# Performance work log

Measured on AMD Instinct MI355X. Metric: run time of the kernel, lower is better.

The kernel has to match this reference:

```python
import jax, jax.numpy as jnp
import numpy as np
from jax.scipy.linalg import expm

B, T = 32, 4096
FREQ_DIM = 128
HID = 64
OUT_DIM = 2
N_COMP = 4
DT = 0.1
EPS = 1e-5


def setup_inputs() -> dict:
    key = jax.random.key(0)
    ks = jax.random.split(key, 16)
    f32 = jnp.float32

    def lin(k, out_d, in_d):
        bound = 1.0 / np.sqrt(in_d)
        kw, kb = jax.random.split(k)
        W = jax.random.uniform(kw, (out_d, in_d), f32, -bound, bound)
        b = jax.random.uniform(kb, (out_d,), f32, -bound, bound)
        return W, b

    x = jax.random.normal(ks[0], (B, T, 1), f32)
    # EnhancedWavePhysics params
    freq_spectrum = jnp.linspace(1.0, 20.0, FREQ_DIM, dtype=f32)
    pm_w1, pm_b1 = lin(ks[1], 128, 1)
    pm_w2, pm_b2 = lin(ks[2], FREQ_DIM * 2, 128)
    wc_w, wc_b = lin(ks[3], HID, FREQ_DIM)
    amp_ctrl = jnp.ones((1,), f32) * 0.1
    # quantum encoder
    qe_w1, qe_b1 = lin(ks[4], HID * 2, HID)
    qe_w2, qe_b2 = lin(ks[5], HID * 4, HID * 2)
    # layernorm
    ln_g = jnp.ones((HID * 4,), f32)
    ln_b = jnp.zeros((HID * 4,), f32)
    # skew-symmetric hamiltonians [4, 64, 64]
    A = jax.random.normal(ks[6], (N_COMP, HID, HID), f32) * 0.05
    hams = (A - jnp.swapaxes(A, -1, -2)) / 2.0
    # interference net
    int_w1, int_b1 = lin(ks[7], 32, 4)
    int_w2, int_b2 = lin(ks[8], OUT_DIM, 32)
    int_strength = jnp.ones((1,), f32)
    return dict(x=x, freq_spectrum=freq_spectrum, pm_w1=pm_w1, pm_b1=pm_b1,
                pm_w2=pm_w2, pm_b2=pm_b2, wc_w=wc_w, wc_b=wc_b,
                amp_ctrl=amp_ctrl, qe_w1=qe_w1, qe_b1=qe_b1, qe_w2=qe_w2,
                qe_b2=qe_b2, ln_g=ln_g, ln_b=ln_b, hams=hams,
                int_w1=int_w1, int_b1=int_b1, int_w2=int_w2, int_b2=int_b2,
                int_strength=int_strength)


def reference(x, freq_spectrum, pm_w1, pm_b1, pm_w2, pm_b2, wc_w, wc_b,
              amp_ctrl, qe_w1, qe_b1, qe_w2, qe_b2, ln_g, ln_b, hams,
              int_w1, int_b1, int_w2, int_b2, int_strength):
    Bx, Tx, _ = x.shape
    # --- EnhancedWavePhysics ---
    mod = jnp.tanh(x @ pm_w1.T + pm_b1) @ pm_w2.T + pm_b2            # [B,T,2F]
    amplitude, phase = jnp.split(mod, 2, axis=-1)                     # [B,T,F]
    amplitude = jnp.tanh(amplitude) * amp_ctrl
    time = jnp.linspace(0.0, 2.0 * np.pi, Tx)[None, :, None]          # [1,T,1]
    freqs = freq_spectrum[None, None, :]                              # [1,1,F]
    wave_components = amplitude * jnp.sin(freqs * time + phase)       # [B,T,F]
    wave_field = jnp.tanh(wave_components @ wc_w.T + wc_b)            # [B,T,H]
    # --- quantum encoder + layernorm ---
    q = jnp.tanh(wave_field @ qe_w1.T + qe_b1) @ qe_w2.T + qe_b2      # [B,T,4H]
    mu = q.mean(-1, keepdims=True)
    var = q.var(-1, keepdims=True)
    q = (q - mu) / jnp.sqrt(var + EPS) * ln_g + ln_b
    psi = q.reshape(Bx, Tx, N_COMP, HID)                              # [B,T,C,D]
    # --- Hamiltonian evolution: torch does matrix_exp(-1j*(1j*H)*dt)=expm(H*dt)
    #     (H skew-symmetric real => U real orthogonal), then psi @ U.T, take real.
    U = jax.vmap(expm)(hams * DT)                                     # [C,D,D]
    evolved = jnp.einsum('btcd,ced->btce', psi, U)                    # [B,T,C,D]
    # --- EnhancedInterference ---
    spec = jnp.abs(jnp.fft.fft(evolved, axis=1))                      # [B,T,C,D]
    freq_w = jax.nn.softmax(spec.mean(-1), axis=1)                    # [B,T,C]
    weighted = jnp.sum(spec * freq_w[..., None], axis=1)              # [B,C,D]
    spatial_avg = weighted.mean(-1)                                   # [B,C]
    out = jnp.tanh(spatial_avg @ int_w1.T + int_b1) @ int_w2.T + int_b2
    return out * int_strength                                         # [B,out_dim]
```

## Files before the change

kernel.cpp:

```cpp
#include <hip/hip_runtime.h>
#include <hip/hip_bf16.h>

#define TT 4096
#define BB 32

typedef unsigned short ushort_t;
typedef __attribute__((ext_vector_type(8))) short short8v;
typedef __attribute__((ext_vector_type(4))) float float4v;

__device__ inline ushort_t bf16rn(float v) {
    unsigned u = __float_as_uint(v);
    unsigned r = (u + 0x7FFFu + ((u >> 16) & 1u)) >> 16;
    return (ushort_t)r;
}
__device__ inline float bf16tof(ushort_t h) {
    return __uint_as_float(((unsigned)h) << 16);
}
__device__ inline int SW(int i) { return i + (i >> 5); }

__device__ inline float fast_tanh(float x) {
    float e = __builtin_amdgcn_exp2f(x * 2.8853900817779268f);
    return 1.0f - 2.0f * __builtin_amdgcn_rcpf(e + 1.0f);
}
__device__ inline float fast_sin(float x) {
    return __builtin_amdgcn_sinf(x * 0.15915494309189535f);
}

__global__ __launch_bounds__(256) void k1_expm(const float* __restrict__ hams,
                                               float* __restrict__ U)
{
    int c = blockIdx.x, tid = threadIdx.x;
    __shared__ float M[4096], P[4096], Acc[4096];
    const float* H = hams + c * 4096;
    for (int k = tid; k < 4096; k += 256) {
        float m = H[k] * 0.1f;
        M[k] = m; P[k] = m;
        Acc[k] = m + (((k >> 6) == (k & 63)) ? 1.0f : 0.0f);
    }
    __syncthreads();
    int j = tid & 63;
    float mcol[64];
    #pragma unroll
    for (int k = 0; k < 64; k++) mcol[k] = M[k * 64 + j];
    for (int term = 2; term <= 8; term++) {
        float inv = 1.0f / (float)term;
        float np_[16];
        #pragma unroll
        for (int r = 0; r < 16; r++) {
            int i = (tid >> 6) + 4 * r;
            float a = 0.f;
            #pragma unroll
            for (int k = 0; k < 64; k++) a = fmaf(P[i * 64 + k], mcol[k], a);
            np_[r] = a * inv;
        }
        __syncthreads();
        #pragma unroll
        for (int r = 0; r < 16; r++) {
            int i = (tid >> 6) + 4 * r;
            P[i * 64 + j] = np_[r];
            Acc[i * 64 + j] += np_[r];
        }
        __syncthreads();
    }
    for (int k = tid; k < 4096; k += 256) U[c * 4096 + k] = Acc[k];
}

__global__ void split_all(const float* __restrict__ pw2, const float* __restrict__ wcw,
                          const float* __restrict__ qw1, const float* __restrict__ qw2,
                          ushort_t* __restrict__ wb)
{
    int i = blockIdx.x * 256 + threadIdx.x;
    const float* src; ushort_t *hi, *lo; int off;
    if (i < 32768)      { src = pw2; hi = wb;          lo = wb + 32768;  off = i; }
    else if (i < 40960) { src = wcw; hi = wb + 65536;  lo = wb + 73728;  off = i - 32768; }
    else if (i < 49152) { src = qw1; hi = wb + 81920;  lo = wb + 90112;  off = i - 40960; }
    else                { src = qw2; hi = wb + 98304;  lo = wb + 131072; off = i - 49152; }
    float v = src[off];
    ushort_t h = bf16rn(v);
    hi[off] = h;
    lo[off] = bf16rn(v - bf16tof(h));
}

template<int EPI>
__global__ __launch_bounds__(256, 2) void gemm_v2(
    const ushort_t* __restrict__ Ahi, const ushort_t* __restrict__ Alo,
    const ushort_t* __restrict__ Whi, const ushort_t* __restrict__ Wlo,
    const float* __restrict__ bias,
    const float* __restrict__ x, const float* __restrict__ pw1,
    const float* __restrict__ pb1,
    const float* __restrict__ freq, const float* __restrict__ ampc,
    const float* __restrict__ lng, const float* __restrict__ lnb,
    ushort_t* __restrict__ OHi, ushort_t* __restrict__ OLo,
    float* __restrict__ OF)
{
    __shared__ float partS[2][4][16], partSS[2][4][16];
    int tid = threadIdx.x;
    int w = tid >> 6, l = tid & 63, l15 = l & 15, kg = l >> 4;
    int kofb = kg * 8;

    short8v bh[4][4], bl[4][4];
    #pragma unroll
    for (int i = 0; i < 4; i++) {
        int n = (w + 4 * i) * 16 + l15;
        #pragma unroll
        for (int kc = 0; kc < 4; kc++) {
            int kof = kc * 32 + kofb;
            bh[i][kc] = *(const short8v*)(Whi + (size_t)n * 128 + kof);
            bl[i][kc] = *(const short8v*)(Wlo + (size_t)n * 128 + kof);
        }
    }

    float fr[2], ba[2], bp[2], am = 0.f;
    float bv[4], g4[4], be4[4];
    if (EPI == 1) {
        am = ampc[0];
        #pragma unroll
        for (int i = 0; i < 2; i++) {
            int f = (w + 4 * i) * 16 + l15;
            fr[i] = freq[f]; ba[i] = bias[f]; bp[i] = bias[128 + f];
        }
    } else {
        #pragma unroll
        for (int i = 0; i < 4; i++) {
            int n = (w + 4 * i) * 16 + l15;
            bv[i] = bias[n]; g4[i] = lng[n]; be4[i] = lnb[n];
        }
    }

    int mbase = blockIdx.x * 64;
    for (int mi = 0; mi < 4; mi++) {
        int m0 = mbase + mi * 16;
        short8v ah[4], al[4];
        if (EPI == 1) {
            float xv = x[m0 + l15];
            #pragma unroll
            for (int kc = 0; kc < 4; kc++) {
                int k0 = kc * 32 + kofb;
                float4 w0 = *(const float4*)(pw1 + k0);
                float4 w1v = *(const float4*)(pw1 + k0 + 4);
                float4 b0 = *(const float4*)(pb1 + k0);
                float4 b1v = *(const float4*)(pb1 + k0 + 4);
                #pragma unroll
                for (int j = 0; j < 8; j++) {
                    float wj = (j < 4) ? (&w0.x)[j] : (&w1v.x)[j - 4];
                    float bj = (j < 4) ? (&b0.x)[j] : (&b1v.x)[j - 4];
                    float v = fast_tanh(fmaf(xv, wj, bj));
                    ushort_t h = bf16rn(v);
                    ah[kc][j] = (short)h;
                    al[kc][j] = (short)bf16rn(v - bf16tof(h));
                }
            }
        } else {
            #pragma unroll
            for (int kc = 0; kc < 4; kc++) {
                int kof = kc * 32 + kofb;
                ah[kc] = *(const short8v*)(Ahi + (size_t)(m0 + l15) * 128 + kof);
                al[kc] = *(const short8v*)(Alo + (size_t)(m0 + l15) * 128 + kof);
            }
        }

        float4v acc[4];
        #pragma unroll
        for (int i = 0; i < 4; i++) acc[i] = (float4v){0.f, 0.f, 0.f, 0.f};
        #pragma unroll
        for (int kc = 0; kc < 4; kc++) {
            #pragma unroll
            for (int i = 0; i < 4; i++) {
                acc[i] = __builtin_amdgcn_mfma_f32_16x16x32_bf16(ah[kc], bh[i][kc], acc[i], 0, 0, 0);
                acc[i] = __builtin_amdgcn_mfma_f32_16x16x32_bf16(ah[kc], bl[i][kc], acc[i], 0, 0, 0);
                acc[i] = __builtin_amdgcn_mfma_f32_16x16x32_bf16(al[kc], bh[i][kc], acc[i], 0, 0, 0);
            }
        }

        if (EPI == 1) {
            #pragma unroll
            for (int i = 0; i < 2; i++) {
                int f = (w + 4 * i) * 16 + l15;
                #pragma unroll
                for (int r = 0; r < 4; r++) {
                    int m = m0 + kg * 4 + r;
                    float timev = 6.283185307179586f * (float)(m & 4095) / 4095.0f;
                    float a = fast_tanh(acc[i][r] + ba[i]) * am;
                    float ph = acc[i + 2][r] + bp[i];
                    float v = a * fast_sin(fmaf(fr[i], timev, ph));
                    ushort_t h = bf16rn(v);
                    OHi[(size_t)m * 128 + f] = h;
                    OLo[(size_t)m * 128 + f] = bf16rn(v - bf16tof(h));
                }
            }
        } else {
            float s[4] = {0, 0, 0, 0}, ss[4] = {0, 0, 0, 0};
            #pragma unroll
            for (int i = 0; i < 4; i++) {
                #pragma unroll
                for (int r = 0; r < 4; r++) {
                    float v = acc[i][r] + bv[i];
                    s[r] += v; ss[r] += v * v;
                }
            }
            #pragma unroll
            for (int r = 0; r < 4; r++) {
                #pragma unroll
                for (int off = 1; off < 16; off <<= 1) {
                    s[r] += __shfl_xor(s[r], off);
                    ss[r] += __shfl_xor(ss[r], off);
                }
            }
            int pb_ = mi & 1;
            if (l15 == 0) {
                #pragma unroll
                for (int r = 0; r < 4; r++) {
                    partS[pb_][w][kg * 4 + r] = s[r];
                    partSS[pb_][w][kg * 4 + r] = ss[r];
                }
            }
            __syncthreads();
            float mu[4], rstd[4];
            #pragma unroll
            for (int r = 0; r < 4; r++) {
                float ts = 0.f, tss = 0.f;
                #pragma unroll
                for (int wv = 0; wv < 4; wv++) {
                    ts += partS[pb_][wv][kg * 4 + r];
                    tss += partSS[pb_][wv][kg * 4 + r];
                }
                mu[r] = ts * (1.0f / 256.0f);
                float var = tss * (1.0f / 256.0f) - mu[r] * mu[r];
                rstd[r] = rsqrtf(var + 1e-5f);
            }
            int b = m0 >> 12;
            int t0 = (m0 & 4095) + kg * 4;
            unsigned* OU = (unsigned*)OF;
            #pragma unroll
            for (int i = 0; i < 4; i++) {
                int n = (w + 4 * i) * 16 + l15;
                uint4 ov;
                #pragma unroll
                for (int r = 0; r < 4; r++) {
                    float v = (acc[i][r] + bv[i] - mu[r]) * rstd[r] * g4[i] + be4[i];
                    ushort_t h = bf16rn(v);
                    ushort_t lo2 = bf16rn(v - bf16tof(h));
                    (&ov.x)[r] = (unsigned)h | ((unsigned)lo2 << 16);
                }
                *(uint4*)(OU + (((size_t)b * 256 + n) << 12) + t0) = ov;
            }
        }
    }
}

__global__ __launch_bounds__(256, 2) void s23_v2(
    const ushort_t* __restrict__ Ahi, const ushort_t* __restrict__ Alo,
    const ushort_t* __restrict__ W2hi, const ushort_t* __restrict__ W2lo,
    const float* __restrict__ b2,
    const ushort_t* __restrict__ W3hi, const ushort_t* __restrict__ W3lo,
    const float* __restrict__ b3,
    ushort_t* __restrict__ OHi, ushort_t* __restrict__ OLo)
{
    __shared__ unsigned WF[2][16][65];
    int tid = threadIdx.x;
    int w = tid >> 6, l = tid & 63, l15 = l & 15, kg = l >> 4;
    int kofb = kg * 8;

    short8v w2h[4], w2l[4];
    #pragma unroll
    for (int kc = 0; kc < 4; kc++) {
        int n = w * 16 + l15;
        int kof = kc * 32 + kofb;
        w2h[kc] = *(const short8v*)(W2hi + (size_t)n * 128 + kof);
        w2l[kc] = *(const short8v*)(W2lo + (size_t)n * 128 + kof);
    }
    short8v w3h[2][2], w3l[2][2];
    #pragma unroll
    for (int i = 0; i < 2; i++) {
        int n = (w + 4 * i) * 16 + l15;
        #pragma unroll
        for (int kc = 0; kc < 2; kc++) {
            int kof = kc * 32 + kofb;
            w3h[i][kc] = *(const short8v*)(W3hi + (size_t)n * 64 + kof);
            w3l[i][kc] = *(const short8v*)(W3lo + (size_t)n * 64 + kof);
        }
    }
    float b2v = b2[w * 16 + l15];
    float b3v[2];
    #pragma unroll
    for (int i = 0; i < 2; i++) b3v[i] = b3[(w + 4 * i) * 16 + l15];

    int mbase = blockIdx.x * 64;
    for (int mi = 0; mi < 4; mi++) {
        int m0 = mbase + mi * 16;
        short8v ah[4], al[4];
        #pragma unroll
        for (int kc = 0; kc < 4; kc++) {
            int kof = kc * 32 + kofb;
            ah[kc] = *(const short8v*)(Ahi + (size_t)(m0 + l15) * 128 + kof);
            al[kc] = *(const short8v*)(Alo + (size_t)(m0 + l15) * 128 + kof);
        }
        float4v acc1 = (float4v){0.f, 0.f, 0.f, 0.f};
        #pragma unroll
        for (int kc = 0; kc < 4; kc++) {
            acc1 = __builtin_amdgcn_mfma_f32_16x16x32_bf16(ah[kc], w2h[kc], acc1, 0, 0, 0);
            acc1 = __builtin_amdgcn_mfma_f32_16x16x32_bf16(ah[kc], w2l[kc], acc1, 0, 0, 0);
            acc1 = __builtin_amdgcn_mfma_f32_16x16x32_bf16(al[kc], w2h[kc], acc1, 0, 0, 0);
        }
        int buf = mi & 1;
        #pragma unroll
        for (int r = 0; r < 4; r++) {
            float v = fast_tanh(acc1[r] + b2v);
            ushort_t h = bf16rn(v);
            ushort_t lo2 = bf16rn(v - bf16tof(h));
            WF[buf][kg * 4 + r][w * 16 + l15] = (unsigned)h | ((unsigned)lo2 << 16);
        }
        __syncthreads();
        float4v acc2[2];
        acc2[0] = (float4v){0.f, 0.f, 0.f, 0.f};
        acc2[1] = (float4v){0.f, 0.f, 0.f, 0.f};
        #pragma unroll
        for (int kc = 0; kc < 2; kc++) {
            short8v a2h, a2l;
            #pragma unroll
            for (int j = 0; j < 8; j++) {
                unsigned u = WF[buf][l15][kc * 32 + kofb + j];
                a2h[j] = (short)(u & 0xFFFFu);
                a2l[j] = (short)(u >> 16);
            }
            #pragma unroll
            for (int i = 0; i < 2; i++) {
                acc2[i] = __builtin_amdgcn_mfma_f32_16x16x32_bf16(a2h, w3h[i][kc], acc2[i], 0, 0, 0);
                acc2[i] = __builtin_amdgcn_mfma_f32_16x16x32_bf16(a2h, w3l[i][kc], acc2[i], 0, 0, 0);
                acc2[i] = __builtin_amdgcn_mfma_f32_16x16x32_bf16(a2l, w3h[i][kc], acc2[i], 0, 0, 0);
            }
        }
        #pragma unroll
        for (int i = 0; i < 2; i++) {
            int n = (w + 4 * i) * 16 + l15;
            #pragma unroll
            for (int r = 0; r < 4; r++) {
                int m = m0 + kg * 4 + r;
                float v = fast_tanh(acc2[i][r] + b3v[i]);
                ushort_t h = bf16rn(v);
                OHi[(size_t)m * 128 + n] = h;
                OLo[(size_t)m * 128 + n] = bf16rn(v - bf16tof(h));
            }
        }
    }
}

__global__ __launch_bounds__(256) void k3a_mfma(float* __restrict__ psi,
                                                const float* __restrict__ U)
{
    __shared__ unsigned QP[64 * 261];
    int bid = blockIdx.x;
    int b = bid >> 6, c = (bid >> 4) & 3, tc = bid & 15;
    int t0 = tc * 256;
    int tid = threadIdx.x;
    int w = tid >> 6, l = tid & 63;
    int l15 = l & 15, kq = l >> 4;
    size_t gbase = ((size_t)(b * 256 + c * 64)) * TT + t0;
    const unsigned* psiu = (const unsigned*)psi;

    for (int i = 0; i < 16; i++) {
        int r_ = i * 4 + w;
        int t4 = l * 4;
        uint4 v = *(const uint4*)(psiu + gbase + (size_t)r_ * TT + t4);
        QP[r_ * 261 + t4 + 0] = v.x;
        QP[r_ * 261 + t4 + 1] = v.y;
        QP[r_ * 261 + t4 + 2] = v.z;
        QP[r_ * 261 + t4 + 3] = v.w;
    }
    __syncthreads();

    short8v ua_hi[2], ua_lo[2];
    #pragma unroll
    for (int kc = 0; kc < 2; kc++) {
        #pragma unroll
        for (int j = 0; j < 8; j++) {
            float v = U[c * 4096 + (w * 16 + l15) * 64 + kc * 32 + kq * 8 + j];
            ushort_t h = bf16rn(v);
            ua_hi[kc][j] = (short)h;
            ua_lo[kc][j] = (short)bf16rn(v - bf16tof(h));
        }
    }

    for (int nt = 0; nt < 16; nt++) {
        float4v acc = (float4v){0.f, 0.f, 0.f, 0.f};
        #pragma unroll
        for (int kc = 0; kc < 2; kc++) {
            short8v b_hi, b_lo;
            #pragma unroll
            for (int j = 0; j < 8; j++) {
                unsigned u = QP[(kc * 32 + kq * 8 + j) * 261 + nt * 16 + l15];
                b_hi[j] = (short)(u & 0xFFFFu);
                b_lo[j] = (short)(u >> 16);
            }
            acc = __builtin_amdgcn_mfma_f32_16x16x32_bf16(ua_hi[kc], b_hi, acc, 0, 0, 0);
            acc = __builtin_amdgcn_mfma_f32_16x16x32_bf16(ua_hi[kc], b_lo, acc, 0, 0, 0);
            acc = __builtin_amdgcn_mfma_f32_16x16x32_bf16(ua_lo[kc], b_hi, acc, 0, 0, 0);
        }
        #pragma unroll
        for (int r = 0; r < 4; r++) {
            int e = w * 16 + kq * 4 + r;
            psi[gbase + (size_t)e * TT + nt * 16 + l15] = acc[r];
        }
    }
}

__global__ __launch_bounds__(256, 2) void k3b_fft(const float* __restrict__ ev,
                                                  float* __restrict__ msum8)
{
    __shared__ float re[4224], im[4224];
    int b = blockIdx.x, c = blockIdx.y, g = blockIdx.z;
    int tid = threadIdx.x;

    float macc[8];
    #pragma unroll
    for (int r = 0; r < 8; r++) macc[r] = 0.f;
    float macc8 = 0.f;

    size_t base = (((size_t)b * 4 + c) * 64 + (size_t)g * 8) * TT;
    for (int p = 0; p < 4; p++) {
        __syncthreads();
        for (int r = 0; r < 4; r++) {
            int t0 = (r * 256 + tid) * 4;
            float4 va = *(const float4*)(ev + base + (size_t)(2 * p) * TT + t0);
            float4 vb = *(const float4*)(ev + base + (size_t)(2 * p + 1) * TT + t0);
            #pragma unroll
            for (int j = 0; j < 4; j++) {
                int rv = __brev((unsigned)(t0 + j)) >> 20;
                re[SW(rv)] = (&va.x)[j];
                im[SW(rv)] = (&vb.x)[j];
            }
        }
        __syncthreads();

        #pragma unroll
        for (int trip = 0; trip < 3; trip++) {
            const int sh = trip * 4;
            int pos = tid & ((1 << sh) - 1);
            int grp = tid >> sh;
            int i0 = (grp << (sh + 4)) + pos;

            float yr[16], yi[16];
            #pragma unroll
            for (int j = 0; j < 16; j++) {
                int a = SW(i0 + (j << sh));
                yr[j] = re[a]; yi[j] = im[a];
            }
            float ang = -(float)pos / (float)(16 << sh);
            float t1r = __builtin_amdgcn_cosf(ang);
            float t1i = __builtin_amdgcn_sinf(ang);
            float t2r = t1r * t1r - t1i * t1i, t2i = 2.f * t1r * t1i;
            float t4r = t2r * t2r - t2i * t2i, t4i = 2.f * t2r * t2i;
            float t8r = t4r * t4r - t4i * t4i, t8i = 2.f * t4r * t4i;

            #pragma unroll
            for (int m = 0; m < 8; m++) {
                int j0 = 2 * m, j1 = j0 + 1;
                float tr = t8r * yr[j1] - t8i * yi[j1];
                float ti = t8r * yi[j1] + t8i * yr[j1];
                yr[j1] = yr[j0] - tr; yi[j1] = yi[j0] - ti;
                yr[j0] += tr;         yi[j0] += ti;
            }
            #pragma unroll
            for (int bs = 0; bs < 16; bs += 4) {
                {
                    int j0 = bs, j1 = bs + 2;
                    float tr = t4r * yr[j1] - t4i * yi[j1];
                    float ti = t4r * yi[j1] + t4i * yr[j1];
                    yr[j1] = yr[j0] - tr; yi[j1] = yi[j0] - ti;
                    yr[j0] += tr;         yi[j0] += ti;
                }
                {
                    int j0 = bs + 1, j1 = bs + 3;
                    float tr = t4i * yr[j1] + t4r * yi[j1];
                    float ti = t4i * yi[j1] - t4r * yr[j1];
                    yr[j1] = yr[j0] - tr; yi[j1] = yi[j0] - ti;
                    yr[j0] += tr;         yi[j0] += ti;
                }
            }
            {
                float wr = t2r, wi = t2i;
                #pragma unroll
                for (int j = 0; j < 4; j++) {
                    #pragma unroll
                    for (int bs = 0; bs < 16; bs += 8) {
                        int j0 = bs + j, j1 = j0 + 4;
                        float tr = wr * yr[j1] - wi * yi[j1];
                        float ti = wr * yi[j1] + wi * yr[j1];
                        yr[j1] = yr[j0] - tr; yi[j1] = yi[j0] - ti;
                        yr[j0] += tr;         yi[j0] += ti;
                    }
                    float nwr = (wr + wi) * 0.70710678f;
                    float nwi = (wi - wr) * 0.70710678f;
                    wr = nwr; wi = nwi;
                }
            }
            {
                float wr = t1r, wi = t1i;
                #pragma unroll
                for (int j = 0; j < 8; j++) {
                    int j0 = j, j1 = j + 8;
                    float tr = wr * yr[j1] - wi * yi[j1];
                    float ti = wr * yi[j1] + wi * yr[j1];
                    yr[j1] = yr[j0] - tr; yi[j1] = yi[j0] - ti;
                    yr[j0] += tr;         yi[j0] += ti;
                    float nwr = wr * 0.92387953f + wi * 0.38268343f;
                    float nwi = wi * 0.92387953f - wr * 0.38268343f;
                    wr = nwr; wi = nwi;
                }
            }
            #pragma unroll
            for (int j = 0; j < 16; j++) {
                int a = SW(i0 + (j << sh));
                re[a] = yr[j]; im[a] = yi[j];
            }
            __syncthreads();
        }

        for (int r = 0; r < 8; r++) {
            int k = tid + r * 256;
            int mk = (4096 - k) & 4095;
            float rk = re[SW(k)], ik = im[SW(k)];
            float rm = re[SW(mk)], imm = im[SW(mk)];
            float dA1 = rk + rm, dA2 = ik - imm;
            float dB1 = ik + imm, dB2 = rk - rm;
            float magA = 0.5f * sqrtf(dA1 * dA1 + dA2 * dA2);
            float magB = 0.5f * sqrtf(dB1 * dB1 + dB2 * dB2);
            macc[r] += magA + magB;
        }
        if (tid == 0) {
            float rk = re[SW(2048)], ik = im[SW(2048)];
            macc8 += fabsf(rk) + fabsf(ik);
        }
    }
    float* ms = msum8 + (((size_t)b * 4 + c) * 8 + g) * 4096;
    for (int r = 0; r < 8; r++) {
        int k = tid + r * 256;
        ms[k] = macc[r];
        if (k > 0) ms[4096 - k] = macc[r];
    }
    if (tid == 0) ms[2048] = macc8;
}

__global__ __launch_bounds__(256) void k4_softdot(const float* __restrict__ msum8,
                                                  float* __restrict__ sa)
{
    __shared__ float m[4096];
    __shared__ float red[256];
    int bc = blockIdx.x, tid = threadIdx.x;
    const float* ms = msum8 + (size_t)bc * 8 * 4096;
    float lmax = -1e30f;
    for (int k = tid; k < 4096; k += 256) {
        float v = 0.f;
        #pragma unroll
        for (int g = 0; g < 8; g++) v += ms[g * 4096 + k];
        v *= (1.0f / 64.0f);
        m[k] = v;
        lmax = fmaxf(lmax, v);
    }
    red[tid] = lmax; __syncthreads();
    for (int s2 = 128; s2 > 0; s2 >>= 1) {
        if (tid < s2) red[tid] = fmaxf(red[tid], red[tid + s2]);
        __syncthreads();
    }
    float mx = red[0]; __syncthreads();
    float lsum = 0.f, ldot = 0.f;
    for (int k = tid; k < 4096; k += 256) {
        float e = expf(m[k] - mx);
        lsum += e; ldot += e * m[k];
    }
    red[tid] = lsum; __syncthreads();
    for (int s2 = 128; s2 > 0; s2 >>= 1) {
        if (tid < s2) red[tid] += red[tid + s2];
        __syncthreads();
    }
    float tsum = red[0]; __syncthreads();
    red[tid] = ldot; __syncthreads();
    for (int s2 = 128; s2 > 0; s2 >>= 1) {
        if (tid < s2) red[tid] += red[tid + s2];
        __syncthreads();
    }
    if (tid == 0) sa[bc] = red[0] / tsum;
}

__global__ void k5_head(const float* __restrict__ sa,
                        const float* __restrict__ w1, const float* __restrict__ b1,
                        const float* __restrict__ w2, const float* __restrict__ b2,
                        const float* __restrict__ strength,
                        float* __restrict__ out)
{
    int b = threadIdx.x;
    if (b >= 32) return;
    float s0 = sa[b * 4 + 0], s1 = sa[b * 4 + 1];
    float s2 = sa[b * 4 + 2], s3 = sa[b * 4 + 3];
    float h[32];
    #pragma unroll
    for (int j = 0; j < 32; j++)
        h[j] = tanhf(b1[j] + w1[j * 4 + 0] * s0 + w1[j * 4 + 1] * s1 +
                     w1[j * 4 + 2] * s2 + w1[j * 4 + 3] * s3);
    float st = strength[0];
    #pragma unroll
    for (int o = 0; o < 2; o++) {
        float a = b2[o];
        #pragma unroll
        for (int j = 0; j < 32; j++) a = fmaf(w2[o * 32 + j], h[j], a);
        out[b * 2 + o] = a * st;
    }
}

extern "C" void kernel_launch(void* const* d_in, const int* in_sizes, int n_in,
                              void* d_out, int out_size, void* d_ws, size_t ws_size,
                              hipStream_t stream)
{
    const float* x    = (const float*)d_in[0];
    const float* freq = (const float*)d_in[1];
    const float* pw1  = (const float*)d_in[2];
    const float* pb1  = (const float*)d_in[3];
    const float* pw2  = (const float*)d_in[4];
    const float* pb2  = (const float*)d_in[5];
    const float* wcw  = (const float*)d_in[6];
    const float* wcb  = (const float*)d_in[7];
    const float* ampc = (const float*)d_in[8];
    const float* qw1  = (const float*)d_in[9];
    const float* qb1  = (const float*)d_in[10];
    const float* qw2  = (const float*)d_in[11];
    const float* qb2  = (const float*)d_in[12];
    const float* lng  = (const float*)d_in[13];
    const float* lnb  = (const float*)d_in[14];
    const float* hams = (const float*)d_in[15];
    const float* iw1  = (const float*)d_in[16];
    const float* ib1  = (const float*)d_in[17];
    const float* iw2  = (const float*)d_in[18];
    const float* ib2  = (const float*)d_in[19];
    const float* istr = (const float*)d_in[20];

    char* wsb = (char*)d_ws;
    ushort_t* AHi = (ushort_t*)(wsb + 0);
    ushort_t* ALo = (ushort_t*)(wsb + 33554432);
    ushort_t* BHi = (ushort_t*)(wsb + 67108864);
    ushort_t* BLo = (ushort_t*)(wsb + 100663296);
    float*    psi = (float*)(wsb + 67108864);
    float*    msum8 = (float*)(wsb + 0);
    float*    U    = (float*)(wsb + 201326592);
    float*    sa   = (float*)(wsb + 201392128);
    ushort_t* wb   = (ushort_t*)(wsb + 203489792);
    ushort_t *pw2hi = wb,          *pw2lo = wb + 32768;
    ushort_t *wcwhi = wb + 65536,  *wcwlo = wb + 73728;
    ushort_t *qw1hi = wb + 81920,  *qw1lo = wb + 90112;
    ushort_t *qw2hi = wb + 98304,  *qw2lo = wb + 131072;
    float* out = (float*)d_out;

    k1_expm<<<4, 256, 0, stream>>>(hams, U);
    split_all<<<320, 256, 0, stream>>>(pw2, wcw, qw1, qw2, wb);

    gemm_v2<1><<<2048, 256, 0, stream>>>(
        (const ushort_t*)nullptr, (const ushort_t*)nullptr, pw2hi, pw2lo, pb2,
        x, pw1, pb1, freq, ampc, (const float*)nullptr, (const float*)nullptr,
        BHi, BLo, (float*)nullptr);
    s23_v2<<<2048, 256, 0, stream>>>(BHi, BLo, wcwhi, wcwlo, wcb,
        qw1hi, qw1lo, qb1, AHi, ALo);
    gemm_v2<2><<<2048, 256, 0, stream>>>(
        AHi, ALo, qw2hi, qw2lo, qb2,
        (const float*)nullptr, (const float*)nullptr, (const float*)nullptr,
        (const float*)nullptr, (const float*)nullptr, lng, lnb,
        (ushort_t*)nullptr, (ushort_t*)nullptr, psi);

    k3a_mfma<<<2048, 256, 0, stream>>>(psi, U);
    k3b_fft<<<dim3(32, 4, 8), 256, 0, stream>>>(psi, msum8);
    k4_softdot<<<128, 256, 0, stream>>>(msum8, sa);
    k5_head<<<1, 64, 0, stream>>>(sa, iw1, ib1, iw2, ib2, istr, out);
}
```

Baseline: 362.4 us.

## Stage GEMM outputs through LDS for coalesced stores and drop lo plane of wave field

The templated gemm_v2 is split into gemm_s1 and gemm_s4. Stage-1 and stage-2/3 outputs are written to shared-memory tiles and then flushed with 16-byte coalesced stores, replacing scattered 2-byte stores. The wave field is now kept only as a single bf16 plane, which removes one global write and read stream and one of the three MFMA passes in s23. The LayerNorm stage transposes its psi tile through LDS so each thread stores contiguous runs along T. The cost is some precision loss on the wave field and a large LDS footprint in gemm_s4 that may limit occupancy.

```diff
diff --git a/kernel.cpp b/kernel.cpp
--- a/kernel.cpp
+++ b/kernel.cpp
@@ -81,19 +81,15 @@
     lo[off] = bf16rn(v - bf16tof(h));
 }
 
-template<int EPI>
-__global__ __launch_bounds__(256, 2) void gemm_v2(
-    const ushort_t* __restrict__ Ahi, const ushort_t* __restrict__ Alo,
+__global__ __launch_bounds__(256, 2) void gemm_s1(
     const ushort_t* __restrict__ Whi, const ushort_t* __restrict__ Wlo,
     const float* __restrict__ bias,
     const float* __restrict__ x, const float* __restrict__ pw1,
     const float* __restrict__ pb1,
     const float* __restrict__ freq, const float* __restrict__ ampc,
-    const float* __restrict__ lng, const float* __restrict__ lnb,
-    ushort_t* __restrict__ OHi, ushort_t* __restrict__ OLo,
-    float* __restrict__ OF)
-{
-    __shared__ float partS[2][4][16], partSS[2][4][16];
+    ushort_t* __restrict__ O)
+{
+    __shared__ ushort_t OT[2][2048];
     int tid = threadIdx.x;
     int w = tid >> 6, l = tid & 63, l15 = l & 15, kg = l >> 4;
     int kofb = kg * 8;
@@ -109,56 +105,36 @@
             bl[i][kc] = *(const short8v*)(Wlo + (size_t)n * 128 + kof);
         }
     }
-
-    float fr[2], ba[2], bp[2], am = 0.f;
-    float bv[4], g4[4], be4[4];
-    if (EPI == 1) {
-        am = ampc[0];
-        #pragma unroll
-        for (int i = 0; i < 2; i++) {
-            int f = (w + 4 * i) * 16 + l15;
-            fr[i] = freq[f]; ba[i] = bias[f]; bp[i] = bias[128 + f];
-        }
-    } else {
-        #pragma unroll
-        for (int i = 0; i < 4; i++) {
-            int n = (w + 4 * i) * 16 + l15;
-            bv[i] = bias[n]; g4[i] = lng[n]; be4[i] = lnb[n];
-        }
+    float am = ampc[0];
+    float fr[2], ba[2], bp[2];
+    #pragma unroll
+    for (int i = 0; i < 2; i++) {
+        int f = (w + 4 * i) * 16 + l15;
+        fr[i] = freq[f]; ba[i] = bias[f]; bp[i] = bias[128 + f];
     }
 
     int mbase = blockIdx.x * 64;
     for (int mi = 0; mi < 4; mi++) {
         int m0 = mbase + mi * 16;
+        float xv = x[m0 + l15];
         short8v ah[4], al[4];
-        if (EPI == 1) {
-            float xv = x[m0 + l15];
-            #pragma unroll
-            for (int kc = 0; kc < 4; kc++) {
-                int k0 = kc * 32 + kofb;
-                float4 w0 = *(const float4*)(pw1 + k0);
-                float4 w1v = *(const float4*)(pw1 + k0 + 4);
-                float4 b0 = *(const float4*)(pb1 + k0);
-                float4 b1v = *(const float4*)(pb1 + k0 + 4);
-                #pragma unroll
-                for (int j = 0; j < 8; j++) {
-                    float wj = (j < 4) ? (&w0.x)[j] : (&w1v.x)[j - 4];
-                    float bj = (j < 4) ? (&b0.x)[j] : (&b1v.x)[j - 4];
-                    float v = fast_tanh(fmaf(xv, wj, bj));
-                    ushort_t h = bf16rn(v);
-                    ah[kc][j] = (short)h;
-                    al[kc][j] = (short)bf16rn(v - bf16tof(h));
-                }
-            }
-        } else {
-            #pragma unroll
-            for (int kc = 0; kc < 4; kc++) {
-                int kof = kc * 32 + kofb;
-                ah[kc] = *(const short8v*)(Ahi + (size_t)(m0 + l15) * 128 + kof);
-                al[kc] = *(const short8v*)(Alo + (size_t)(m0 + l15) * 128 + kof);
-            }
-        }
-
+        #pragma unroll
+        for (int kc = 0; kc < 4; kc++) {
+            int k0 = kc * 32 + kofb;
+            float4 w0 = *(const float4*)(pw1 + k0);
+            float4 w1v = *(const float4*)(pw1 + k0 + 4);
+            float4 b0 = *(const float4*)(pb1 + k0);
+            float4 b1v = *(const float4*)(pb1 + k0 + 4);
+            #pragma unroll
+            for (int j = 0; j < 8; j++) {
+                float wj = (j < 4) ? (&w0.x)[j] : (&w1v.x)[j - 4];
+                float bj = (j < 4) ? (&b0.x)[j] : (&b1v.x)[j - 4];
+                float v = fast_tanh(fmaf(xv, wj, bj));
+                ushort_t h = bf16rn(v);
+                ah[kc][j] = (short)h;
+                al[kc][j] = (short)bf16rn(v - bf16tof(h));
+            }
+        }
         float4v acc[4];
         #pragma unroll
         for (int i = 0; i < 4; i++) acc[i] = (float4v){0.f, 0.f, 0.f, 0.f};
@@ -171,85 +147,27 @@
                 acc[i] = __builtin_amdgcn_mfma_f32_16x16x32_bf16(al[kc], bh[i][kc], acc[i], 0, 0, 0);
             }
         }
-
-        if (EPI == 1) {
-            #pragma unroll
-            for (int i = 0; i < 2; i++) {
-                int f = (w + 4 * i) * 16 + l15;
-                #pragma unroll
-                for (int r = 0; r < 4; r++) {
-                    int m = m0 + kg * 4 + r;
-                    float timev = 6.283185307179586f * (float)(m & 4095) / 4095.0f;
-                    float a = fast_tanh(acc[i][r] + ba[i]) * am;
-                    float ph = acc[i + 2][r] + bp[i];
-                    float v = a * fast_sin(fmaf(fr[i], timev, ph));
-                    ushort_t h = bf16rn(v);
-                    OHi[(size_t)m * 128 + f] = h;
-                    OLo[(size_t)m * 128 + f] = bf16rn(v - bf16tof(h));
-                }
-            }
-        } else {
-            float s[4] = {0, 0, 0, 0}, ss[4] = {0, 0, 0, 0};
-            #pragma unroll
-            for (int i = 0; i < 4; i++) {
-                #pragma unroll
-                for (int r = 0; r < 4; r++) {
-                    float v = acc[i][r] + bv[i];
-                    s[r] += v; ss[r] += v * v;
-                }
-            }
+        int buf = mi & 1;
+        #pragma unroll
+        for (int i = 0; i < 2; i++) {
+            int f = (w + 4 * i) * 16 + l15;
             #pragma unroll
             for (int r = 0; r < 4; r++) {
-                #pragma unroll
-                for (int off = 1; off < 16; off <<= 1) {
-                    s[r] += __shfl_xor(s[r], off);
-                    ss[r] += __shfl_xor(ss[r], off);
-                }
-            }
-            int pb_ = mi & 1;
-            if (l15 == 0) {
-                #pragma unroll
-                for (int r = 0; r < 4; r++) {
-                    partS[pb_][w][kg * 4 + r] = s[r];
-                    partSS[pb_][w][kg * 4 + r] = ss[r];
-                }
-            }
-            __syncthreads();
-            float mu[4], rstd[4];
-            #pragma unroll
-            for (int r = 0; r < 4; r++) {
-                float ts = 0.f, tss = 0.f;
-                #pragma unroll
-                for (int wv = 0; wv < 4; wv++) {
-                    ts += partS[pb_][wv][kg * 4 + r];
-                    tss += partSS[pb_][wv][kg * 4 + r];
-                }
-                mu[r] = ts * (1.0f / 256.0f);
-                float var = tss * (1.0f / 256.0f) - mu[r] * mu[r];
-                rstd[r] = rsqrtf(var + 1e-5f);
-            }
-            int b = m0 >> 12;
-            int t0 = (m0 & 4095) + kg * 4;
-            unsigned* OU = (unsigned*)OF;
-            #pragma unroll
-            for (int i = 0; i < 4; i++) {
-                int n = (w + 4 * i) * 16 + l15;
-                uint4 ov;
-                #pragma unroll
-                for (int r = 0; r < 4; r++) {
-                    float v = (acc[i][r] + bv[i] - mu[r]) * rstd[r] * g4[i] + be4[i];
-                    ushort_t h = bf16rn(v);
-                    ushort_t lo2 = bf16rn(v - bf16tof(h));
-                    (&ov.x)[r] = (unsigned)h | ((unsigned)lo2 << 16);
-                }
-                *(uint4*)(OU + (((size_t)b * 256 + n) << 12) + t0) = ov;
-            }
-        }
+                int m = m0 + kg * 4 + r;
+                float timev = 6.283185307179586f * (float)(m & 4095) / 4095.0f;
+                float a = fast_tanh(acc[i][r] + ba[i]) * am;
+                float ph = acc[i + 2][r] + bp[i];
+                float v = a * fast_sin(fmaf(fr[i], timev, ph));
+                OT[buf][(kg * 4 + r) * 128 + f] = bf16rn(v);
+            }
+        }
+        __syncthreads();
+        *(uint4*)(O + (size_t)m0 * 128 + tid * 8) = *(const uint4*)(&OT[buf][tid * 8]);
     }
 }
 
 __global__ __launch_bounds__(256, 2) void s23_v2(
-    const ushort_t* __restrict__ Ahi, const ushort_t* __restrict__ Alo,
+    const ushort_t* __restrict__ A,
     const ushort_t* __restrict__ W2hi, const ushort_t* __restrict__ W2lo,
     const float* __restrict__ b2,
     const ushort_t* __restrict__ W3hi, const ushort_t* __restrict__ W3lo,
@@ -257,6 +175,7 @@
     ushort_t* __restrict__ OHi, ushort_t* __restrict__ OLo)
 {
     __shared__ unsigned WF[2][16][65];
+    __shared__ ushort_t OThi[2][2048], OTlo[2][2048];
     int tid = threadIdx.x;
     int w = tid >> 6, l = tid & 63, l15 = l & 15, kg = l >> 4;
     int kofb = kg * 8;
@@ -288,19 +207,17 @@
     int mbase = blockIdx.x * 64;
     for (int mi = 0; mi < 4; mi++) {
         int m0 = mbase + mi * 16;
-        short8v ah[4], al[4];
+        short8v ah[4];
         #pragma unroll
         for (int kc = 0; kc < 4; kc++) {
             int kof = kc * 32 + kofb;
-            ah[kc] = *(const short8v*)(Ahi + (size_t)(m0 + l15) * 128 + kof);
-            al[kc] = *(const short8v*)(Alo + (size_t)(m0 + l15) * 128 + kof);
+            ah[kc] = *(const short8v*)(A + (size_t)(m0 + l15) * 128 + kof);
         }
         float4v acc1 = (float4v){0.f, 0.f, 0.f, 0.f};
         #pragma unroll
         for (int kc = 0; kc < 4; kc++) {
             acc1 = __builtin_amdgcn_mfma_f32_16x16x32_bf16(ah[kc], w2h[kc], acc1, 0, 0, 0);
             acc1 = __builtin_amdgcn_mfma_f32_16x16x32_bf16(ah[kc], w2l[kc], acc1, 0, 0, 0);
-            acc1 = __builtin_amdgcn_mfma_f32_16x16x32_bf16(al[kc], w2h[kc], acc1, 0, 0, 0);
         }
         int buf = mi & 1;
         #pragma unroll
@@ -335,13 +252,134 @@
             int n = (w + 4 * i) * 16 + l15;
             #pragma unroll
             for (int r = 0; r < 4; r++) {
-                int m = m0 + kg * 4 + r;
                 float v = fast_tanh(acc2[i][r] + b3v[i]);
                 ushort_t h = bf16rn(v);
-                OHi[(size_t)m * 128 + n] = h;
-                OLo[(size_t)m * 128 + n] = bf16rn(v - bf16tof(h));
-            }
-        }
+                OThi[buf][(kg * 4 + r) * 128 + n] = h;
+                OTlo[buf][(kg * 4 + r) * 128 + n] = bf16rn(v - bf16tof(h));
+            }
+        }
+        __syncthreads();
+        *(uint4*)(OHi + (size_t)m0 * 128 + tid * 8) = *(const uint4*)(&OThi[buf][tid * 8]);
+        *(uint4*)(OLo + (size_t)m0 * 128 + tid * 8) = *(const uint4*)(&OTlo[buf][tid * 8]);
+    }
+}
+
+__global__ __launch_bounds__(256, 2) void gemm_s4(
+    const ushort_t* __restrict__ Ahi, const ushort_t* __restrict__ Alo,
+    const ushort_t* __restrict__ Whi, const ushort_t* __restrict__ Wlo,
+    const float* __restrict__ bias,
+    const float* __restrict__ lng, const float* __restrict__ lnb,
+    unsigned* __restrict__ psiu)
+{
+    __shared__ float partS[2][4][16], partSS[2][4][16];
+    __shared__ unsigned PT[256 * 65];
+    int tid = threadIdx.x;
+    int w = tid >> 6, l = tid & 63, l15 = l & 15, kg = l >> 4;
+    int kofb = kg * 8;
+
+    short8v bh[4][4], bl[4][4];
+    #pragma unroll
+    for (int i = 0; i < 4; i++) {
+        int n = (w + 4 * i) * 16 + l15;
+        #pragma unroll
+        for (int kc = 0; kc < 4; kc++) {
+            int kof = kc * 32 + kofb;
+            bh[i][kc] = *(const short8v*)(Whi + (size_t)n * 128 + kof);
+            bl[i][kc] = *(const short8v*)(Wlo + (size_t)n * 128 + kof);
+        }
+    }
+    float bv[4], g4[4], be4[4];
+    #pragma unroll
+    for (int i = 0; i < 4; i++) {
+        int n = (w + 4 * i) * 16 + l15;
+        bv[i] = bias[n]; g4[i] = lng[n]; be4[i] = lnb[n];
+    }
+
+    int mbase = blockIdx.x * 64;
+    int b = mbase >> 12, tbase = mbase & 4095;
+    for (int mi = 0; mi < 4; mi++) {
+        int m0 = mbase + mi * 16;
+        short8v ah[4], al[4];
+        #pragma unroll
+        for (int kc = 0; kc < 4; kc++) {
+            int kof = kc * 32 + kofb;
+            ah[kc] = *(const short8v*)(Ahi + (size_t)(m0 + l15) * 128 + kof);
+            al[kc] = *(const short8v*)(Alo + (size_t)(m0 + l15) * 128 + kof);
+        }
+        float4v acc[4];
+        #pragma unroll
+        for (int i = 0; i < 4; i++) acc[i] = (float4v){0.f, 0.f, 0.f, 0.f};
+        #pragma unroll
+        for (int kc = 0; kc < 4; kc++) {
+            #pragma unroll
+            for (int i = 0; i < 4; i++) {
+                acc[i] = __builtin_amdgcn_mfma_f32_16x16x32_bf16(ah[kc], bh[i][kc], acc[i], 0, 0, 0);
+                acc[i] = __builtin_amdgcn_mfma_f32_16x16x32_bf16(ah[kc], bl[i][kc], acc[i], 0, 0, 0);
+                acc[i] = __builtin_amdgcn_mfma_f32_16x16x32_bf16(al[kc], bh[i][kc], acc[i], 0, 0, 0);
+            }
+        }
+        float s[4] = {0, 0, 0, 0}, ss[4] = {0, 0, 0, 0};
+        #pragma unroll
+        for (int i = 0; i < 4; i++) {
+            #pragma unroll
+            for (int r = 0; r < 4; r++) {
+                float v = acc[i][r] + bv[i];
+                s[r] += v; ss[r] += v * v;
+            }
+        }
+        #pragma unroll
+        for (int r = 0; r < 4; r++) {
+            #pragma unroll
+            for (int off = 1; off < 16; off <<= 1) {
+                s[r] += __shfl_xor(s[r], off);
+                ss[r] += __shfl_xor(ss[r], off);
+            }
+        }
+        int pb_ = mi & 1;
+        if (l15 == 0) {
+            #pragma unroll
+            for (int r = 0; r < 4; r++) {
+                partS[pb_][w][kg * 4 + r] = s[r];
+                partSS[pb_][w][kg * 4 + r] = ss[r];
+            }
+        }
+        __syncthreads();
+        float mu[4], rstd[4];
+        #pragma unroll
+        for (int r = 0; r < 4; r++) {
+            float ts = 0.f, tss = 0.f;
+            #pragma unroll
+            for (int wv = 0; wv < 4; wv++) {
+                ts += partS[pb_][wv][kg * 4 + r];
+                tss += partSS[pb_][wv][kg * 4 + r];
+            }
+            mu[r] = ts * (1.0f / 256.0f);
+            float var = tss * (1.0f / 256.0f) - mu[r] * mu[r];
+            rstd[r] = rsqrtf(var + 1e-5f);
+        }
+        #pragma unroll
+        for (int i = 0; i < 4; i++) {
+            int n = (w + 4 * i) * 16 + l15;
+            #pragma unroll
+            for (int r = 0; r < 4; r++) {
+                float v = (acc[i][r] + bv[i] - mu[r]) * rstd[r] * g4[i] + be4[i];
+                ushort_t h = bf16rn(v);
+                ushort_t lo2 = bf16rn(v - bf16tof(h));
+                PT[n * 65 + mi * 16 + kg * 4 + r] = (unsigned)h | ((unsigned)lo2 << 16);
+            }
+        }
+    }
+    __syncthreads();
+    int n = tid;
+    size_t gb = ((size_t)(b * 256 + n)) * 4096 + tbase;
+    #pragma unroll
+    for (int j = 0; j < 16; j++) {
+        uint4 v;
+        v.x = PT[n * 65 + j * 4 + 0];
+        v.y = PT[n * 65 + j * 4 + 1];
+        v.z = PT[n * 65 + j * 4 + 2];
+        v.w = PT[n * 65 + j * 4 + 3];
+        *(uint4*)(psiu + gb + j * 4) = v;
     }
 }
 
@@ -636,8 +674,7 @@
     char* wsb = (char*)d_ws;
     ushort_t* AHi = (ushort_t*)(wsb + 0);
     ushort_t* ALo = (ushort_t*)(wsb + 33554432);
-    ushort_t* BHi = (ushort_t*)(wsb + 67108864);
-    ushort_t* BLo = (ushort_t*)(wsb + 100663296);
+    ushort_t* Bwcf = (ushort_t*)(wsb + 67108864);
     float*    psi = (float*)(wsb + 67108864);
     float*    msum8 = (float*)(wsb + 0);
     float*    U    = (float*)(wsb + 201326592);
@@ -652,17 +689,12 @@
     k1_expm<<<4, 256, 0, stream>>>(hams, U);
     split_all<<<320, 256, 0, stream>>>(pw2, wcw, qw1, qw2, wb);
 
-    gemm_v2<1><<<2048, 256, 0, stream>>>(
-        (const ushort_t*)nullptr, (const ushort_t*)nullptr, pw2hi, pw2lo, pb2,
-        x, pw1, pb1, freq, ampc, (const float*)nullptr, (const float*)nullptr,
-        BHi, BLo, (float*)nullptr);
-    s23_v2<<<2048, 256, 0, stream>>>(BHi, BLo, wcwhi, wcwlo, wcb,
+    gemm_s1<<<2048, 256, 0, stream>>>(pw2hi, pw2lo, pb2, x, pw1, pb1,
+                                      freq, ampc, Bwcf);
+    s23_v2<<<2048, 256, 0, stream>>>(Bwcf, wcwhi, wcwlo, wcb,
         qw1hi, qw1lo, qb1, AHi, ALo);
-    gemm_v2<2><<<2048, 256, 0, stream>>>(
-        AHi, ALo, qw2hi, qw2lo, qb2,
-        (const float*)nullptr, (const float*)nullptr, (const float*)nullptr,
-        (const float*)nullptr, (const float*)nullptr, lng, lnb,
-        (ushort_t*)nullptr, (ushort_t*)nullptr, psi);
+    gemm_s4<<<2048, 256, 0, stream>>>(AHi, ALo, qw2hi, qw2lo, qb2,
+        lng, lnb, (unsigned*)psi);
 
     k3a_mfma<<<2048, 256, 0, stream>>>(psi, U);
     k3b_fft<<<dim3(32, 4, 8), 256, 0, stream>>>(psi, msum8);
```

Result: no change. 365.6 us (+0.9%).
